# Performance work log

Measured on AMD Instinct MI355X. Metric: run time of the kernel, lower is better.

## Reference

```python
import jax, jax.numpy as jnp
import numpy as np

TEMPERATURE = 0.1
THRESHOLD = 0.2
EPS = 1e-12


def setup_inputs() -> dict:
    key = jax.random.key(0)
    k0, k1 = jax.random.split(key)
    f0 = jax.random.normal(k0, (1, 256, 80, 80), dtype=jnp.float32)
    f1 = jax.random.normal(k1, (1, 256, 80, 80), dtype=jnp.float32)
    return {"f0": f0, "f1": f1}


def reference(f0, f1):
    B, C, H0, W0 = f0.shape
    _, _, H1, W1 = f1.shape
    N0, N1 = H0 * W0, H1 * W1

    # (B, N, C), L2-normalized along C (matches F.normalize with eps clamp)
    f0_flat = f0.reshape(B, C, N0).transpose(0, 2, 1)
    f1_flat = f1.reshape(B, C, N1).transpose(0, 2, 1)
    f0n = f0_flat / jnp.maximum(jnp.linalg.norm(f0_flat, axis=-1, keepdims=True), EPS)
    f1n = f1_flat / jnp.maximum(jnp.linalg.norm(f1_flat, axis=-1, keepdims=True), EPS)

    # cosine similarity / temperature: (B, N0, N1)
    S = jnp.einsum('bnc,bmc->bnm', f0n, f1n) / TEMPERATURE
    # dual softmax
    P = jax.nn.softmax(S, axis=-1) * jax.nn.softmax(S, axis=-2)

    # mutual nearest-neighbor matching (B == 1 branch)
    conf = jnp.max(P[0], axis=-1)              # (N0,)
    indices0 = jnp.argmax(P[0], axis=-1)       # (N0,) row argmax
    indices1 = jnp.argmax(P[0], axis=-2)       # (N1,) column argmax
    ar0 = jnp.arange(N0)
    mutual = indices1[indices0] == ar0
    valid = mutual & (conf > THRESHOLD)        # (N0,) bool

    # fixed-shape (jit-friendly) match outputs: full grid, zeroed where invalid
    mkpts0 = jnp.stack([ar0 % W0, ar0 // W0], axis=1).astype(jnp.float32)
    mkpts1 = jnp.stack([indices0 % W1, indices0 // W1], axis=1).astype(jnp.float32)
    vf = valid[:, None].astype(jnp.float32)
    mkpts0 = mkpts0 * vf
    mkpts1 = mkpts1 * vf
    mconf = jnp.where(valid, conf, 0.0)

    return (P, mkpts0, mkpts1, mconf, valid)
```

## Files before the change

kernel.cpp:

```cpp
#include <hip/hip_runtime.h>

#define N0 6400
#define NC 256
#define WW 80

using half8   = __attribute__((ext_vector_type(8))) _Float16;
using floatx4 = __attribute__((ext_vector_type(4))) float;
#define GLOBAL_AS __attribute__((address_space(1)))
#define LDS_AS    __attribute__((address_space(3)))

__device__ __forceinline__ unsigned long long packvi(float v, int i) {
    return ((unsigned long long)__float_as_uint(v) << 32) | (unsigned int)i;
}

__global__ __launch_bounds__(256) void knorm(const float* __restrict__ f0,
                                             const float* __restrict__ f1,
                                             float* __restrict__ snorm,
                                             float* __restrict__ rowsum,
                                             float* __restrict__ colsum,
                                             unsigned long long* __restrict__ rowbest,
                                             unsigned long long* __restrict__ colbest) {
    int g = blockIdx.x * 256 + threadIdx.x;
    if (g < N0) {
        rowsum[g] = 0.f; colsum[g] = 0.f;
        rowbest[g] = 0ull; colbest[g] = 0ull;
    }
    int h = (g >= 12800) ? 1 : 0;
    int j = g - h * 12800;
    const float* src = (j < N0) ? f0 : f1;
    int n = (j < N0) ? j : (j - N0);
    int c0 = h * 128;
    float s = 0.f;
#pragma unroll 8
    for (int c = 0; c < 128; ++c) {
        float v = src[(c0 + c) * N0 + n];
        s += v * v;
    }
    snorm[g] = s;
}

__global__ __launch_bounds__(256) void ktrans(const float* __restrict__ f0,
                                              const float* __restrict__ f1,
                                              const float* __restrict__ snorm,
                                              _Float16* __restrict__ A2,
                                              _Float16* __restrict__ B2) {
    __shared__ float tile[32][33];
    const float* src = blockIdx.z ? f1 : f0;
    _Float16* dst    = blockIdx.z ? B2 : A2;
    int t = threadIdx.x;
    int n0 = blockIdx.x * 32, c0 = blockIdx.y * 32;
    int tx = t & 31, ty = t >> 5;
#pragma unroll
    for (int u = 0; u < 4; ++u)
        tile[ty + u * 8][tx] = src[(c0 + ty + u * 8) * N0 + n0 + tx];
    __syncthreads();
    int row = t >> 3;
    int cg  = (t & 7) * 4;
    int n = n0 + row;
    int j = (blockIdx.z ? N0 : 0) + n;
    float s = snorm[j] + snorm[12800 + j];
    float iv = 1.0f / fmaxf(sqrtf(s), 1e-12f);
    union { ushort4 u4; _Float16 h[4]; } pk;
#pragma unroll
    for (int u = 0; u < 4; ++u)
        pk.h[u] = (_Float16)(tile[cg + u][row] * iv);
    *(ushort4*)&dst[n * NC + c0 + cg] = pk.u4;
}

__device__ __forceinline__ void stage_chunk(const _Float16* __restrict__ G,
                                            unsigned short* lds, int r0, int kc,
                                            int tid) {
    int rl = tid >> 3;
    int ch = ((tid & 7) ^ (rl & 7)) * 8;
#pragma unroll
    for (int kk = 0; kk < 2; ++kk)
#pragma unroll
        for (int g = 0; g < 4; ++g) {
            const _Float16* ga = G + (r0 + g * 32 + rl) * NC + kc * 128 + kk * 64 + ch;
            __builtin_amdgcn_global_load_lds((const GLOBAL_AS unsigned int*)ga,
                (LDS_AS unsigned int*)&lds[kk * 8192 + g * 2048 + tid * 8], 16, 0, 0);
        }
}

template<bool HI>
__device__ __forceinline__ void compute_half(const unsigned short* bbuf,
                                             const unsigned short* abufHi,
                                             const half8 aflo[4][4],
                                             int lane, int wm, int wn,
                                             floatx4 acc[4][4]) {
    int q = lane >> 4;
#pragma unroll
    for (int s = 0; s < 4; ++s) {
        int c = s * 4 + q, kk = c >> 3, cq = c & 7;
        half8 af[4], bf[4];
#pragma unroll
        for (int mt = 0; mt < 4; ++mt) {
            int rb = wn * 64 + mt * 16 + (lane & 15);
            bf[mt] = *(const half8*)&bbuf[kk * 8192 + rb * 64 + ((cq ^ (rb & 7)) * 8)];
        }
#pragma unroll
        for (int mt = 0; mt < 4; ++mt) {
            if (HI) {
                int ra = wm * 64 + mt * 16 + (lane & 15);
                af[mt] = *(const half8*)&abufHi[kk * 8192 + ra * 64 + ((cq ^ (ra & 7)) * 8)];
            } else {
                af[mt] = aflo[mt][s];
            }
        }
#pragma unroll
        for (int mt = 0; mt < 4; ++mt)
#pragma unroll
            for (int nt = 0; nt < 4; ++nt)
                acc[mt][nt] = __builtin_amdgcn_mfma_f32_16x16x32_f16(
                    af[mt], bf[nt], acc[mt][nt], 0, 0, 0);
    }
}

__global__ __launch_bounds__(256, 2) void kgemm1(const _Float16* __restrict__ A2,
                                                 const _Float16* __restrict__ B2,
                                                 float* __restrict__ rowsum,
                                                 float* __restrict__ colsum) {
    __shared__ __align__(16) unsigned short lds[32768];
    unsigned short* regA = lds;
    unsigned short* regB = lds + 16384;
    int tid = threadIdx.x, lane = tid & 63, wave = tid >> 6;
    int wm = wave & 1, wn = wave >> 1, q = lane >> 4;
    int i0 = blockIdx.x * 128, jp = blockIdx.y * 640;

    stage_chunk(A2, regB, i0, 0, tid);
    stage_chunk(A2, regA, i0, 1, tid);
    __syncthreads();
    half8 aflo[4][4];
#pragma unroll
    for (int mt = 0; mt < 4; ++mt)
#pragma unroll
        for (int s = 0; s < 4; ++s) {
            int c = s * 4 + q, kk = c >> 3, cq = c & 7;
            int ra = wm * 64 + mt * 16 + (lane & 15);
            aflo[mt][s] = *(const half8*)&regB[kk * 8192 + ra * 64 + ((cq ^ (ra & 7)) * 8)];
        }
    __syncthreads();

    float rsum[4][4] = {};

    for (int jt = 0; jt < 5; ++jt) {
        stage_chunk(B2, regB, jp + jt * 128, 0, tid);
        __syncthreads();
        floatx4 acc[4][4] = {};
        compute_half<false>(regB, regA, aflo, lane, wm, wn, acc);
        __syncthreads();
        stage_chunk(B2, regB, jp + jt * 128, 1, tid);
        __syncthreads();
        compute_half<true>(regB, regA, aflo, lane, wm, wn, acc);

        float csum[4] = {0.f, 0.f, 0.f, 0.f};
#pragma unroll
        for (int mt = 0; mt < 4; ++mt)
#pragma unroll
            for (int r = 0; r < 4; ++r) {
                float rv = 0.f;
#pragma unroll
                for (int nt = 0; nt < 4; ++nt) {
                    float e = __expf(10.0f * acc[mt][nt][r]);
                    rv += e; csum[nt] += e;
                }
                rsum[mt][r] += rv;
            }
#pragma unroll
        for (int nt = 0; nt < 4; ++nt) {
            csum[nt] += __shfl_xor(csum[nt], 16);
            csum[nt] += __shfl_xor(csum[nt], 32);
        }
        if (lane < 16)
#pragma unroll
            for (int nt = 0; nt < 4; ++nt)
                atomicAdd(&colsum[jp + jt * 128 + wn * 64 + nt * 16 + lane], csum[nt]);
        __syncthreads();
    }
#pragma unroll
    for (int mt = 0; mt < 4; ++mt)
#pragma unroll
        for (int r = 0; r < 4; ++r) {
            float v = rsum[mt][r];
            v += __shfl_xor(v, 1);
            v += __shfl_xor(v, 2);
            v += __shfl_xor(v, 4);
            v += __shfl_xor(v, 8);
            if ((lane & 15) == 0)
                atomicAdd(&rowsum[i0 + wm * 64 + mt * 16 + q * 4 + r], v);
        }
}

__global__ __launch_bounds__(256, 2) void kgemm2(const _Float16* __restrict__ A2,
                                                 const _Float16* __restrict__ B2,
                                                 const float* __restrict__ rowsum,
                                                 const float* __restrict__ colsum,
                                                 float* __restrict__ P,
                                                 unsigned long long* __restrict__ rowbest,
                                                 unsigned long long* __restrict__ colbest) {
    __shared__ __align__(16) unsigned short lds[32768];
    unsigned short* regA = lds;
    unsigned short* regB = lds + 16384;
    int tid = threadIdx.x, lane = tid & 63, wave = tid >> 6;
    int wm = wave & 1, wn = wave >> 1, q = lane >> 4;
    int i0 = blockIdx.x * 128, jp = blockIdx.y * 640;

    stage_chunk(A2, regB, i0, 0, tid);
    stage_chunk(A2, regA, i0, 1, tid);
    __syncthreads();
    half8 aflo[4][4];
#pragma unroll
    for (int mt = 0; mt < 4; ++mt)
#pragma unroll
        for (int s = 0; s < 4; ++s) {
            int c = s * 4 + q, kk = c >> 3, cq = c & 7;
            int ra = wm * 64 + mt * 16 + (lane & 15);
            aflo[mt][s] = *(const half8*)&regB[kk * 8192 + ra * 64 + ((cq ^ (ra & 7)) * 8)];
        }
    __syncthreads();

    float ir[4][4];
#pragma unroll
    for (int mt = 0; mt < 4; ++mt) {
        float4 v4 = *(const float4*)&rowsum[i0 + wm * 64 + mt * 16 + q * 4];
        ir[mt][0] = 1.0f / v4.x; ir[mt][1] = 1.0f / v4.y;
        ir[mt][2] = 1.0f / v4.z; ir[mt][3] = 1.0f / v4.w;
    }

    unsigned long long rbv[4][4] = {};

    for (int jt = 0; jt < 5; ++jt) {
        stage_chunk(B2, regB, jp + jt * 128, 0, tid);
        __syncthreads();
        floatx4 acc[4][4] = {};
        compute_half<false>(regB, regA, aflo, lane, wm, wn, acc);
        __syncthreads();
        stage_chunk(B2, regB, jp + jt * 128, 1, tid);
        __syncthreads();
        compute_half<true>(regB, regA, aflo, lane, wm, wn, acc);

        int cb0 = jp + jt * 128 + wn * 64 + (lane & 15);
        float ic[4];
#pragma unroll
        for (int nt = 0; nt < 4; ++nt) ic[nt] = 1.0f / colsum[cb0 + nt * 16];

        unsigned long long colb[4] = {0ull, 0ull, 0ull, 0ull};
#pragma unroll
        for (int mt = 0; mt < 4; ++mt) {
            int rb0 = i0 + wm * 64 + mt * 16 + q * 4;
#pragma unroll
            for (int r = 0; r < 4; ++r) {
                int row = rb0 + r;
#pragma unroll
                for (int nt = 0; nt < 4; ++nt) {
                    float pv = __expf(20.0f * acc[mt][nt][r]) * ir[mt][r] * ic[nt];
                    P[row * N0 + cb0 + nt * 16] = pv;
                    unsigned long long pr = packvi(pv, cb0 + nt * 16);
                    if (pr > rbv[mt][r]) rbv[mt][r] = pr;
                    unsigned long long pc = packvi(pv, row);
                    if (pc > colb[nt]) colb[nt] = pc;
                }
            }
        }
#pragma unroll
        for (int nt = 0; nt < 4; ++nt) {
            unsigned long long o = __shfl_xor(colb[nt], 16);
            if (o > colb[nt]) colb[nt] = o;
            o = __shfl_xor(colb[nt], 32);
            if (o > colb[nt]) colb[nt] = o;
        }
        if (lane < 16)
#pragma unroll
            for (int nt = 0; nt < 4; ++nt)
                atomicMax(&colbest[cb0 + nt * 16], colb[nt]);
        __syncthreads();
    }
#pragma unroll
    for (int mt = 0; mt < 4; ++mt)
#pragma unroll
        for (int r = 0; r < 4; ++r) {
            unsigned long long v = rbv[mt][r];
#pragma unroll
            for (int s = 1; s < 16; s <<= 1) {
                unsigned long long o = __shfl_xor(v, s);
                if (o > v) v = o;
            }
            if ((lane & 15) == 0)
                atomicMax(&rowbest[i0 + wm * 64 + mt * 16 + q * 4 + r], v);
        }
}

__global__ __launch_bounds__(256) void kmatch(const unsigned long long* __restrict__ rowbest,
                                              const unsigned long long* __restrict__ colbest,
                                              float* __restrict__ out) {
    int i = blockIdx.x * 256 + threadIdx.x;
    unsigned long long rb = rowbest[i];
    float conf = __uint_as_float((unsigned int)(rb >> 32));
    int jj = (int)(rb & 0xffffffffu);
    unsigned long long cb = colbest[jj];
    int i2 = (int)(cb & 0xffffffffu);
    bool valid = (i2 == i) && (conf > 0.2f);
    float vf = valid ? 1.0f : 0.0f;

    float* mk0   = out + 40960000;
    float* mk1   = out + 40972800;
    float* mconf = out + 40985600;
    float* vout  = out + 40992000;
    mk0[i * 2 + 0] = vf * (float)(i % WW);
    mk0[i * 2 + 1] = vf * (float)(i / WW);
    mk1[i * 2 + 0] = vf * (float)(jj % WW);
    mk1[i * 2 + 1] = vf * (float)(jj / WW);
    mconf[i] = valid ? conf : 0.0f;
    vout[i]  = vf;
}

extern "C" void kernel_launch(void* const* d_in, const int* in_sizes, int n_in,
                              void* d_out, int out_size, void* d_ws, size_t ws_size,
                              hipStream_t stream) {
    const float* f0 = (const float*)d_in[0];
    const float* f1 = (const float*)d_in[1];
    float* out = (float*)d_out;

    _Float16* A2 = (_Float16*)d_ws;
    _Float16* B2 = A2 + 6400 * 256;
    float* snorm  = (float*)(B2 + 6400 * 256);
    float* rowsum = snorm + 25600;
    float* colsum = rowsum + 6400;
    unsigned long long* rowbest = (unsigned long long*)(colsum + 6400);
    unsigned long long* colbest = rowbest + 6400;

    knorm<<<100, 256, 0, stream>>>(f0, f1, snorm,
                                   rowsum, colsum, rowbest, colbest);
    ktrans<<<dim3(200, 8, 2), 256, 0, stream>>>(f0, f1, snorm, A2, B2);
    kgemm1<<<dim3(50, 10), 256, 0, stream>>>(A2, B2, rowsum, colsum);
    kgemm2<<<dim3(50, 10), 256, 0, stream>>>(A2, B2, rowsum, colsum,
                                             out, rowbest, colbest);
    kmatch<<<25, 256, 0, stream>>>(rowbest, colbest, out);
}
```

Baseline: 280.9 us.

## Replace global atomics with per-block partial buffers and a separate reduce pass

Instead of atomicAdd/atomicMax into shared row/col accumulators, each GEMM block reduces within LDS across its waves and writes its own partials to workspace. A small kreduce kernel sums the partials, and the match kernel takes the max over them. The P stores also switch to nontemporal. This removes atomic contention, but it adds an extra launch, extra partial-buffer traffic, and a 50-way strided gather per row in the match kernel. It depends on the workspace being large enough and falls back to the old atomic path otherwise.

```diff
diff --git a/kernel.cpp b/kernel.cpp
--- a/kernel.cpp
+++ b/kernel.cpp
@@ -116,33 +116,43 @@
     }
 }
 
-__global__ __launch_bounds__(256, 2) void kgemm1(const _Float16* __restrict__ A2,
-                                                 const _Float16* __restrict__ B2,
-                                                 float* __restrict__ rowsum,
-                                                 float* __restrict__ colsum) {
+__device__ __forceinline__ void gemm_prologue(const _Float16* __restrict__ A2,
+                                              unsigned short* regA,
+                                              unsigned short* regB,
+                                              int i0, int tid, int lane,
+                                              int wm, half8 aflo[4][4]) {
+    int q = lane >> 4;
+    stage_chunk(A2, regB, i0, 0, tid);
+    stage_chunk(A2, regA, i0, 1, tid);
+    __syncthreads();
+#pragma unroll
+    for (int mt = 0; mt < 4; ++mt)
+#pragma unroll
+        for (int s = 0; s < 4; ++s) {
+            int c = s * 4 + q, kk = c >> 3, cq = c & 7;
+            int ra = wm * 64 + mt * 16 + (lane & 15);
+            aflo[mt][s] = *(const half8*)&regB[kk * 8192 + ra * 64 + ((cq ^ (ra & 7)) * 8)];
+        }
+    __syncthreads();
+}
+
+__global__ __launch_bounds__(256, 2) void kgemm1P(const _Float16* __restrict__ A2,
+                                                  const _Float16* __restrict__ B2,
+                                                  float* __restrict__ rowpart,
+                                                  float* __restrict__ colpart) {
     __shared__ __align__(16) unsigned short lds[32768];
+    __shared__ float cs[2][128];
+    __shared__ float rs[2][128];
     unsigned short* regA = lds;
     unsigned short* regB = lds + 16384;
     int tid = threadIdx.x, lane = tid & 63, wave = tid >> 6;
     int wm = wave & 1, wn = wave >> 1, q = lane >> 4;
     int i0 = blockIdx.x * 128, jp = blockIdx.y * 640;
 
-    stage_chunk(A2, regB, i0, 0, tid);
-    stage_chunk(A2, regA, i0, 1, tid);
-    __syncthreads();
     half8 aflo[4][4];
-#pragma unroll
-    for (int mt = 0; mt < 4; ++mt)
-#pragma unroll
-        for (int s = 0; s < 4; ++s) {
-            int c = s * 4 + q, kk = c >> 3, cq = c & 7;
-            int ra = wm * 64 + mt * 16 + (lane & 15);
-            aflo[mt][s] = *(const half8*)&regB[kk * 8192 + ra * 64 + ((cq ^ (ra & 7)) * 8)];
-        }
-    __syncthreads();
+    gemm_prologue(A2, regA, regB, i0, tid, lane, wm, aflo);
 
     float rsum[4][4] = {};
-
     for (int jt = 0; jt < 5; ++jt) {
         stage_chunk(B2, regB, jp + jt * 128, 0, tid);
         __syncthreads();
@@ -174,8 +184,10 @@
         if (lane < 16)
 #pragma unroll
             for (int nt = 0; nt < 4; ++nt)
-                atomicAdd(&colsum[jp + jt * 128 + wn * 64 + nt * 16 + lane], csum[nt]);
-        __syncthreads();
+                cs[wm][wn * 64 + nt * 16 + lane] = csum[nt];
+        __syncthreads();
+        if (tid < 128)
+            colpart[blockIdx.x * N0 + jp + jt * 128 + tid] = cs[0][tid] + cs[1][tid];
     }
 #pragma unroll
     for (int mt = 0; mt < 4; ++mt)
@@ -187,37 +199,50 @@
             v += __shfl_xor(v, 4);
             v += __shfl_xor(v, 8);
             if ((lane & 15) == 0)
-                atomicAdd(&rowsum[i0 + wm * 64 + mt * 16 + q * 4 + r], v);
-        }
-}
-
-__global__ __launch_bounds__(256, 2) void kgemm2(const _Float16* __restrict__ A2,
-                                                 const _Float16* __restrict__ B2,
-                                                 const float* __restrict__ rowsum,
-                                                 const float* __restrict__ colsum,
-                                                 float* __restrict__ P,
-                                                 unsigned long long* __restrict__ rowbest,
-                                                 unsigned long long* __restrict__ colbest) {
+                rs[wn][wm * 64 + mt * 16 + q * 4 + r] = v;
+        }
+    __syncthreads();
+    if (tid < 128)
+        rowpart[blockIdx.y * N0 + i0 + tid] = rs[0][tid] + rs[1][tid];
+}
+
+__global__ __launch_bounds__(256) void kreduce(const float* __restrict__ rowpart,
+                                               const float* __restrict__ colpart,
+                                               float* __restrict__ rowsum,
+                                               float* __restrict__ colsum) {
+    int t = blockIdx.x * 256 + threadIdx.x;
+    if (t < N0) {
+        float s = 0.f;
+#pragma unroll
+        for (int y = 0; y < 10; ++y) s += rowpart[y * N0 + t];
+        rowsum[t] = s;
+    } else {
+        int j = t - N0;
+        float s = 0.f;
+#pragma unroll
+        for (int x = 0; x < 50; ++x) s += colpart[x * N0 + j];
+        colsum[j] = s;
+    }
+}
+
+__global__ __launch_bounds__(256, 2) void kgemm2P(const _Float16* __restrict__ A2,
+                                                  const _Float16* __restrict__ B2,
+                                                  const float* __restrict__ rowsum,
+                                                  const float* __restrict__ colsum,
+                                                  float* __restrict__ P,
+                                                  unsigned long long* __restrict__ rowbpart,
+                                                  unsigned long long* __restrict__ colbpart) {
     __shared__ __align__(16) unsigned short lds[32768];
+    __shared__ unsigned long long cbst[2][128];
+    __shared__ unsigned long long rbst[2][128];
     unsigned short* regA = lds;
     unsigned short* regB = lds + 16384;
     int tid = threadIdx.x, lane = tid & 63, wave = tid >> 6;
     int wm = wave & 1, wn = wave >> 1, q = lane >> 4;
     int i0 = blockIdx.x * 128, jp = blockIdx.y * 640;
 
-    stage_chunk(A2, regB, i0, 0, tid);
-    stage_chunk(A2, regA, i0, 1, tid);
-    __syncthreads();
     half8 aflo[4][4];
-#pragma unroll
-    for (int mt = 0; mt < 4; ++mt)
-#pragma unroll
-        for (int s = 0; s < 4; ++s) {
-            int c = s * 4 + q, kk = c >> 3, cq = c & 7;
-            int ra = wm * 64 + mt * 16 + (lane & 15);
-            aflo[mt][s] = *(const half8*)&regB[kk * 8192 + ra * 64 + ((cq ^ (ra & 7)) * 8)];
-        }
-    __syncthreads();
+    gemm_prologue(A2, regA, regB, i0, tid, lane, wm, aflo);
 
     float ir[4][4];
 #pragma unroll
@@ -228,7 +253,6 @@
     }
 
     unsigned long long rbv[4][4] = {};
-
     for (int jt = 0; jt < 5; ++jt) {
         stage_chunk(B2, regB, jp + jt * 128, 0, tid);
         __syncthreads();
@@ -254,7 +278,7 @@
 #pragma unroll
                 for (int nt = 0; nt < 4; ++nt) {
                     float pv = __expf(20.0f * acc[mt][nt][r]) * ir[mt][r] * ic[nt];
-                    P[row * N0 + cb0 + nt * 16] = pv;
+                    __builtin_nontemporal_store(pv, &P[row * N0 + cb0 + nt * 16]);
                     unsigned long long pr = packvi(pv, cb0 + nt * 16);
                     if (pr > rbv[mt][r]) rbv[mt][r] = pr;
                     unsigned long long pc = packvi(pv, row);
@@ -272,8 +296,12 @@
         if (lane < 16)
 #pragma unroll
             for (int nt = 0; nt < 4; ++nt)
-                atomicMax(&colbest[cb0 + nt * 16], colb[nt]);
-        __syncthreads();
+                cbst[wm][wn * 64 + nt * 16 + lane] = colb[nt];
+        __syncthreads();
+        if (tid < 128) {
+            unsigned long long a = cbst[0][tid], b = cbst[1][tid];
+            colbpart[blockIdx.x * N0 + jp + jt * 128 + tid] = (a > b) ? a : b;
+        }
     }
 #pragma unroll
     for (int mt = 0; mt < 4; ++mt)
@@ -286,18 +314,32 @@
                 if (o > v) v = o;
             }
             if ((lane & 15) == 0)
-                atomicMax(&rowbest[i0 + wm * 64 + mt * 16 + q * 4 + r], v);
-        }
-}
-
-__global__ __launch_bounds__(256) void kmatch(const unsigned long long* __restrict__ rowbest,
-                                              const unsigned long long* __restrict__ colbest,
-                                              float* __restrict__ out) {
+                rbst[wn][wm * 64 + mt * 16 + q * 4 + r] = v;
+        }
+    __syncthreads();
+    if (tid < 128) {
+        unsigned long long a = rbst[0][tid], b = rbst[1][tid];
+        rowbpart[blockIdx.y * N0 + i0 + tid] = (a > b) ? a : b;
+    }
+}
+
+__global__ __launch_bounds__(256) void kmatchP(const unsigned long long* __restrict__ rowbpart,
+                                               const unsigned long long* __restrict__ colbpart,
+                                               float* __restrict__ out) {
     int i = blockIdx.x * 256 + threadIdx.x;
-    unsigned long long rb = rowbest[i];
+    unsigned long long rb = 0ull;
+#pragma unroll
+    for (int y = 0; y < 10; ++y) {
+        unsigned long long v = rowbpart[y * N0 + i];
+        if (v > rb) rb = v;
+    }
     float conf = __uint_as_float((unsigned int)(rb >> 32));
     int jj = (int)(rb & 0xffffffffu);
-    unsigned long long cb = colbest[jj];
+    unsigned long long cb = 0ull;
+    for (int x = 0; x < 50; ++x) {
+        unsigned long long v = colbpart[x * N0 + jj];
+        if (v > cb) cb = v;
+    }
     int i2 = (int)(cb & 0xffffffffu);
     bool valid = (i2 == i) && (conf > 0.2f);
     float vf = valid ? 1.0f : 0.0f;
@@ -314,6 +356,180 @@
     vout[i]  = vf;
 }
 
+__global__ __launch_bounds__(256, 2) void kgemm1A(const _Float16* __restrict__ A2,
+                                                  const _Float16* __restrict__ B2,
+                                                  float* __restrict__ rowsum,
+                                                  float* __restrict__ colsum) {
+    __shared__ __align__(16) unsigned short lds[32768];
+    unsigned short* regA = lds;
+    unsigned short* regB = lds + 16384;
+    int tid = threadIdx.x, lane = tid & 63, wave = tid >> 6;
+    int wm = wave & 1, wn = wave >> 1, q = lane >> 4;
+    int i0 = blockIdx.x * 128, jp = blockIdx.y * 640;
+
+    half8 aflo[4][4];
+    gemm_prologue(A2, regA, regB, i0, tid, lane, wm, aflo);
+
+    float rsum[4][4] = {};
+    for (int jt = 0; jt < 5; ++jt) {
+        stage_chunk(B2, regB, jp + jt * 128, 0, tid);
+        __syncthreads();
+        floatx4 acc[4][4] = {};
+        compute_half<false>(regB, regA, aflo, lane, wm, wn, acc);
+        __syncthreads();
+        stage_chunk(B2, regB, jp + jt * 128, 1, tid);
+        __syncthreads();
+        compute_half<true>(regB, regA, aflo, lane, wm, wn, acc);
+
+        float csum[4] = {0.f, 0.f, 0.f, 0.f};
+#pragma unroll
+        for (int mt = 0; mt < 4; ++mt)
+#pragma unroll
+            for (int r = 0; r < 4; ++r) {
+                float rv = 0.f;
+#pragma unroll
+                for (int nt = 0; nt < 4; ++nt) {
+                    float e = __expf(10.0f * acc[mt][nt][r]);
+                    rv += e; csum[nt] += e;
+                }
+                rsum[mt][r] += rv;
+            }
+#pragma unroll
+        for (int nt = 0; nt < 4; ++nt) {
+            csum[nt] += __shfl_xor(csum[nt], 16);
+            csum[nt] += __shfl_xor(csum[nt], 32);
+        }
+        if (lane < 16)
+#pragma unroll
+            for (int nt = 0; nt < 4; ++nt)
+                atomicAdd(&colsum[jp + jt * 128 + wn * 64 + nt * 16 + lane], csum[nt]);
+        __syncthreads();
+    }
+#pragma unroll
+    for (int mt = 0; mt < 4; ++mt)
+#pragma unroll
+        for (int r = 0; r < 4; ++r) {
+            float v = rsum[mt][r];
+            v += __shfl_xor(v, 1);
+            v += __shfl_xor(v, 2);
+            v += __shfl_xor(v, 4);
+            v += __shfl_xor(v, 8);
+            if ((lane & 15) == 0)
+                atomicAdd(&rowsum[i0 + wm * 64 + mt * 16 + q * 4 + r], v);
+        }
+}
+
+__global__ __launch_bounds__(256, 2) void kgemm2A(const _Float16* __restrict__ A2,
+                                                  const _Float16* __restrict__ B2,
+                                                  const float* __restrict__ rowsum,
+                                                  const float* __restrict__ colsum,
+                                                  float* __restrict__ P,
+                                                  unsigned long long* __restrict__ rowbest,
+                                                  unsigned long long* __restrict__ colbest) {
+    __shared__ __align__(16) unsigned short lds[32768];
+    unsigned short* regA = lds;
+    unsigned short* regB = lds + 16384;
+    int tid = threadIdx.x, lane = tid & 63, wave = tid >> 6;
+    int wm = wave & 1, wn = wave >> 1, q = lane >> 4;
+    int i0 = blockIdx.x * 128, jp = blockIdx.y * 640;
+
+    half8 aflo[4][4];
+    gemm_prologue(A2, regA, regB, i0, tid, lane, wm, aflo);
+
+    float ir[4][4];
+#pragma unroll
+    for (int mt = 0; mt < 4; ++mt) {
+        float4 v4 = *(const float4*)&rowsum[i0 + wm * 64 + mt * 16 + q * 4];
+        ir[mt][0] = 1.0f / v4.x; ir[mt][1] = 1.0f / v4.y;
+        ir[mt][2] = 1.0f / v4.z; ir[mt][3] = 1.0f / v4.w;
+    }
+
+    unsigned long long rbv[4][4] = {};
+    for (int jt = 0; jt < 5; ++jt) {
+        stage_chunk(B2, regB, jp + jt * 128, 0, tid);
+        __syncthreads();
+        floatx4 acc[4][4] = {};
+        compute_half<false>(regB, regA, aflo, lane, wm, wn, acc);
+        __syncthreads();
+        stage_chunk(B2, regB, jp + jt * 128, 1, tid);
+        __syncthreads();
+        compute_half<true>(regB, regA, aflo, lane, wm, wn, acc);
+
+        int cb0 = jp + jt * 128 + wn * 64 + (lane & 15);
+        float ic[4];
+#pragma unroll
+        for (int nt = 0; nt < 4; ++nt) ic[nt] = 1.0f / colsum[cb0 + nt * 16];
+
+        unsigned long long colb[4] = {0ull, 0ull, 0ull, 0ull};
+#pragma unroll
+        for (int mt = 0; mt < 4; ++mt) {
+            int rb0 = i0 + wm * 64 + mt * 16 + q * 4;
+#pragma unroll
+            for (int r = 0; r < 4; ++r) {
+                int row = rb0 + r;
+#pragma unroll
+                for (int nt = 0; nt < 4; ++nt) {
+                    float pv = __expf(20.0f * acc[mt][nt][r]) * ir[mt][r] * ic[nt];
+                    P[row * N0 + cb0 + nt * 16] = pv;
+                    unsigned long long pr = packvi(pv, cb0 + nt * 16);
+                    if (pr > rbv[mt][r]) rbv[mt][r] = pr;
+                    unsigned long long pc = packvi(pv, row);
+                    if (pc > colb[nt]) colb[nt] = pc;
+                }
+            }
+        }
+#pragma unroll
+        for (int nt = 0; nt < 4; ++nt) {
+            unsigned long long o = __shfl_xor(colb[nt], 16);
+            if (o > colb[nt]) colb[nt] = o;
+            o = __shfl_xor(colb[nt], 32);
+            if (o > colb[nt]) colb[nt] = o;
+        }
+        if (lane < 16)
+#pragma unroll
+            for (int nt = 0; nt < 4; ++nt)
+                atomicMax(&colbest[cb0 + nt * 16], colb[nt]);
+        __syncthreads();
+    }
+#pragma unroll
+    for (int mt = 0; mt < 4; ++mt)
+#pragma unroll
+        for (int r = 0; r < 4; ++r) {
+            unsigned long long v = rbv[mt][r];
+#pragma unroll
+            for (int s = 1; s < 16; s <<= 1) {
+                unsigned long long o = __shfl_xor(v, s);
+                if (o > v) v = o;
+            }
+            if ((lane & 15) == 0)
+                atomicMax(&rowbest[i0 + wm * 64 + mt * 16 + q * 4 + r], v);
+        }
+}
+
+__global__ __launch_bounds__(256) void kmatchA(const unsigned long long* __restrict__ rowbest,
+                                               const unsigned long long* __restrict__ colbest,
+                                               float* __restrict__ out) {
+    int i = blockIdx.x * 256 + threadIdx.x;
+    unsigned long long rb = rowbest[i];
+    float conf = __uint_as_float((unsigned int)(rb >> 32));
+    int jj = (int)(rb & 0xffffffffu);
+    unsigned long long cb = colbest[jj];
+    int i2 = (int)(cb & 0xffffffffu);
+    bool valid = (i2 == i) && (conf > 0.2f);
+    float vf = valid ? 1.0f : 0.0f;
+
+    float* mk0   = out + 40960000;
+    float* mk1   = out + 40972800;
+    float* mconf = out + 40985600;
+    float* vout  = out + 40992000;
+    mk0[i * 2 + 0] = vf * (float)(i % WW);
+    mk0[i * 2 + 1] = vf * (float)(i / WW);
+    mk1[i * 2 + 0] = vf * (float)(jj % WW);
+    mk1[i * 2 + 1] = vf * (float)(jj / WW);
+    mconf[i] = valid ? conf : 0.0f;
+    vout[i]  = vf;
+}
+
 extern "C" void kernel_launch(void* const* d_in, const int* in_sizes, int n_in,
                               void* d_out, int out_size, void* d_ws, size_t ws_size,
                               hipStream_t stream) {
@@ -323,17 +539,32 @@
 
     _Float16* A2 = (_Float16*)d_ws;
     _Float16* B2 = A2 + 6400 * 256;
-    float* snorm  = (float*)(B2 + 6400 * 256);
-    float* rowsum = snorm + 25600;
-    float* colsum = rowsum + 6400;
+    float* snorm   = (float*)(B2 + 6400 * 256);
+    float* rowsum  = snorm + 25600;
+    float* colsum  = rowsum + 6400;
     unsigned long long* rowbest = (unsigned long long*)(colsum + 6400);
     unsigned long long* colbest = rowbest + 6400;
+    float* rowpart = (float*)(colbest + 6400);
+    float* colpart = rowpart + 10 * 6400;
+    unsigned long long* rowbpart =
+        (unsigned long long*)(colpart + 50 * 6400);
+    unsigned long long* colbpart = rowbpart + 10 * 6400;
+    const size_t WS_NEEDED_P = 11417600;
 
     knorm<<<100, 256, 0, stream>>>(f0, f1, snorm,
                                    rowsum, colsum, rowbest, colbest);
     ktrans<<<dim3(200, 8, 2), 256, 0, stream>>>(f0, f1, snorm, A2, B2);
-    kgemm1<<<dim3(50, 10), 256, 0, stream>>>(A2, B2, rowsum, colsum);
-    kgemm2<<<dim3(50, 10), 256, 0, stream>>>(A2, B2, rowsum, colsum,
-                                             out, rowbest, colbest);
-    kmatch<<<25, 256, 0, stream>>>(rowbest, colbest, out);
-}
+
+    if (ws_size >= WS_NEEDED_P) {
+        kgemm1P<<<dim3(50, 10), 256, 0, stream>>>(A2, B2, rowpart, colpart);
+        kreduce<<<50, 256, 0, stream>>>(rowpart, colpart, rowsum, colsum);
+        kgemm2P<<<dim3(50, 10), 256, 0, stream>>>(A2, B2, rowsum, colsum,
+                                                  out, rowbpart, colbpart);
+        kmatchP<<<25, 256, 0, stream>>>(rowbpart, colbpart, out);
+    } else {
+        kgemm1A<<<dim3(50, 10), 256, 0, stream>>>(A2, B2, rowsum, colsum);
+        kgemm2A<<<dim3(50, 10), 256, 0, stream>>>(A2, B2, rowsum, colsum,
+                                                  out, rowbest, colbest);
+        kmatchA<<<25, 256, 0, stream>>>(rowbest, colbest, out);
+    }
+}
```

Measured after the change: 294.3 us. 4.8% more time.

## Replace global atomics with partial buffers, log-domain argmax, and coalesced P stores

Applied to the files above, without the earlier changes.

Global atomicAdd/atomicMax reductions of row/column sums and best indices are replaced by per-block partial arrays, combined by a new reduce kernel and inside the match kernel. The argmax keys move to the log domain (S plus log normalizers), so P values no longer need packing, and conf is read back from P. The P writes go through a per-wave LDS scratch to form 16-byte coalesced nontemporal stores instead of strided scalar stores. This adds one kernel launch and extra partial-buffer traffic, and log-domain ties could pick a different index than comparing exact P values.

```diff
diff --git a/kernel.cpp b/kernel.cpp
--- a/kernel.cpp
+++ b/kernel.cpp
@@ -15,16 +15,8 @@
 
 __global__ __launch_bounds__(256) void knorm(const float* __restrict__ f0,
                                              const float* __restrict__ f1,
-                                             float* __restrict__ snorm,
-                                             float* __restrict__ rowsum,
-                                             float* __restrict__ colsum,
-                                             unsigned long long* __restrict__ rowbest,
-                                             unsigned long long* __restrict__ colbest) {
+                                             float* __restrict__ snorm) {
     int g = blockIdx.x * 256 + threadIdx.x;
-    if (g < N0) {
-        rowsum[g] = 0.f; colsum[g] = 0.f;
-        rowbest[g] = 0ull; colbest[g] = 0ull;
-    }
     int h = (g >= 12800) ? 1 : 0;
     int j = g - h * 12800;
     const float* src = (j < N0) ? f0 : f1;
@@ -116,33 +108,43 @@
     }
 }
 
-__global__ __launch_bounds__(256, 2) void kgemm1(const _Float16* __restrict__ A2,
-                                                 const _Float16* __restrict__ B2,
-                                                 float* __restrict__ rowsum,
-                                                 float* __restrict__ colsum) {
+__device__ __forceinline__ void gemm_prologue(const _Float16* __restrict__ A2,
+                                              unsigned short* regA,
+                                              unsigned short* regB,
+                                              int i0, int tid, int lane,
+                                              int wm, half8 aflo[4][4]) {
+    int q = lane >> 4;
+    stage_chunk(A2, regB, i0, 0, tid);
+    stage_chunk(A2, regA, i0, 1, tid);
+    __syncthreads();
+#pragma unroll
+    for (int mt = 0; mt < 4; ++mt)
+#pragma unroll
+        for (int s = 0; s < 4; ++s) {
+            int c = s * 4 + q, kk = c >> 3, cq = c & 7;
+            int ra = wm * 64 + mt * 16 + (lane & 15);
+            aflo[mt][s] = *(const half8*)&regB[kk * 8192 + ra * 64 + ((cq ^ (ra & 7)) * 8)];
+        }
+    __syncthreads();
+}
+
+__global__ __launch_bounds__(256, 2) void kgemm1P(const _Float16* __restrict__ A2,
+                                                  const _Float16* __restrict__ B2,
+                                                  float* __restrict__ rowpart,
+                                                  float* __restrict__ colpart) {
     __shared__ __align__(16) unsigned short lds[32768];
+    __shared__ float cs[2][128];
+    __shared__ float rs[2][128];
     unsigned short* regA = lds;
     unsigned short* regB = lds + 16384;
     int tid = threadIdx.x, lane = tid & 63, wave = tid >> 6;
     int wm = wave & 1, wn = wave >> 1, q = lane >> 4;
     int i0 = blockIdx.x * 128, jp = blockIdx.y * 640;
 
-    stage_chunk(A2, regB, i0, 0, tid);
-    stage_chunk(A2, regA, i0, 1, tid);
-    __syncthreads();
     half8 aflo[4][4];
-#pragma unroll
-    for (int mt = 0; mt < 4; ++mt)
-#pragma unroll
-        for (int s = 0; s < 4; ++s) {
-            int c = s * 4 + q, kk = c >> 3, cq = c & 7;
-            int ra = wm * 64 + mt * 16 + (lane & 15);
-            aflo[mt][s] = *(const half8*)&regB[kk * 8192 + ra * 64 + ((cq ^ (ra & 7)) * 8)];
-        }
-    __syncthreads();
+    gemm_prologue(A2, regA, regB, i0, tid, lane, wm, aflo);
 
     float rsum[4][4] = {};
-
     for (int jt = 0; jt < 5; ++jt) {
         stage_chunk(B2, regB, jp + jt * 128, 0, tid);
         __syncthreads();
@@ -174,8 +176,10 @@
         if (lane < 16)
 #pragma unroll
             for (int nt = 0; nt < 4; ++nt)
-                atomicAdd(&colsum[jp + jt * 128 + wn * 64 + nt * 16 + lane], csum[nt]);
-        __syncthreads();
+                cs[wm][wn * 64 + nt * 16 + lane] = csum[nt];
+        __syncthreads();
+        if (tid < 128)
+            colpart[blockIdx.x * N0 + jp + jt * 128 + tid] = cs[0][tid] + cs[1][tid];
     }
 #pragma unroll
     for (int mt = 0; mt < 4; ++mt)
@@ -187,48 +191,65 @@
             v += __shfl_xor(v, 4);
             v += __shfl_xor(v, 8);
             if ((lane & 15) == 0)
-                atomicAdd(&rowsum[i0 + wm * 64 + mt * 16 + q * 4 + r], v);
-        }
-}
-
-__global__ __launch_bounds__(256, 2) void kgemm2(const _Float16* __restrict__ A2,
-                                                 const _Float16* __restrict__ B2,
-                                                 const float* __restrict__ rowsum,
-                                                 const float* __restrict__ colsum,
-                                                 float* __restrict__ P,
-                                                 unsigned long long* __restrict__ rowbest,
-                                                 unsigned long long* __restrict__ colbest) {
+                rs[wn][wm * 64 + mt * 16 + q * 4 + r] = v;
+        }
+    __syncthreads();
+    if (tid < 128)
+        rowpart[blockIdx.y * N0 + i0 + tid] = rs[0][tid] + rs[1][tid];
+}
+
+__global__ __launch_bounds__(256) void kreduce(const float* __restrict__ rowpart,
+                                               const float* __restrict__ colpart,
+                                               float* __restrict__ rowsum,
+                                               float* __restrict__ colsum) {
+    int t = blockIdx.x * 256 + threadIdx.x;
+    if (t < N0) {
+        float s = 0.f;
+#pragma unroll
+        for (int y = 0; y < 10; ++y) s += rowpart[y * N0 + t];
+        rowsum[t] = s;
+    } else {
+        int j = t - N0;
+        float s = 0.f;
+#pragma unroll
+        for (int x = 0; x < 50; ++x) s += colpart[x * N0 + j];
+        colsum[j] = s;
+    }
+}
+
+__global__ __launch_bounds__(256, 2) void kgemm2P(const _Float16* __restrict__ A2,
+                                                  const _Float16* __restrict__ B2,
+                                                  const float* __restrict__ rowsum,
+                                                  const float* __restrict__ colsum,
+                                                  float* __restrict__ P,
+                                                  unsigned long long* __restrict__ rowbpart,
+                                                  unsigned long long* __restrict__ colbpart) {
     __shared__ __align__(16) unsigned short lds[32768];
+    __shared__ unsigned long long cbst[2][128];
+    __shared__ unsigned long long rbst[2][128];
     unsigned short* regA = lds;
     unsigned short* regB = lds + 16384;
     int tid = threadIdx.x, lane = tid & 63, wave = tid >> 6;
     int wm = wave & 1, wn = wave >> 1, q = lane >> 4;
     int i0 = blockIdx.x * 128, jp = blockIdx.y * 640;
 
-    stage_chunk(A2, regB, i0, 0, tid);
-    stage_chunk(A2, regA, i0, 1, tid);
-    __syncthreads();
     half8 aflo[4][4];
-#pragma unroll
-    for (int mt = 0; mt < 4; ++mt)
-#pragma unroll
-        for (int s = 0; s < 4; ++s) {
-            int c = s * 4 + q, kk = c >> 3, cq = c & 7;
-            int ra = wm * 64 + mt * 16 + (lane & 15);
-            aflo[mt][s] = *(const half8*)&regB[kk * 8192 + ra * 64 + ((cq ^ (ra & 7)) * 8)];
-        }
-    __syncthreads();
-
-    float ir[4][4];
+    gemm_prologue(A2, regA, regB, i0, tid, lane, wm, aflo);
+
+    float ir[4][4], lr[4][4];
 #pragma unroll
     for (int mt = 0; mt < 4; ++mt) {
         float4 v4 = *(const float4*)&rowsum[i0 + wm * 64 + mt * 16 + q * 4];
         ir[mt][0] = 1.0f / v4.x; ir[mt][1] = 1.0f / v4.y;
         ir[mt][2] = 1.0f / v4.z; ir[mt][3] = 1.0f / v4.w;
-    }
+#pragma unroll
+        for (int r = 0; r < 4; ++r)
+            lr[mt][r] = __logf(ir[mt][r]) * 0.05f + 4.0f;
+    }
+
+    float* scr = (float*)lds + 8192 + wave * 1056;
 
     unsigned long long rbv[4][4] = {};
-
     for (int jt = 0; jt < 5; ++jt) {
         stage_chunk(B2, regB, jp + jt * 128, 0, tid);
         __syncthreads();
@@ -239,10 +260,14 @@
         __syncthreads();
         compute_half<true>(regB, regA, aflo, lane, wm, wn, acc);
 
-        int cb0 = jp + jt * 128 + wn * 64 + (lane & 15);
-        float ic[4];
-#pragma unroll
-        for (int nt = 0; nt < 4; ++nt) ic[nt] = 1.0f / colsum[cb0 + nt * 16];
+        int jcb = jp + jt * 128 + wn * 64;
+        int cb0 = jcb + (lane & 15);
+        float ic[4], lc[4];
+#pragma unroll
+        for (int nt = 0; nt < 4; ++nt) {
+            ic[nt] = 1.0f / colsum[cb0 + nt * 16];
+            lc[nt] = __logf(ic[nt]) * 0.05f + 4.0f;
+        }
 
         unsigned long long colb[4] = {0ull, 0ull, 0ull, 0ull};
 #pragma unroll
@@ -251,15 +276,23 @@
 #pragma unroll
             for (int r = 0; r < 4; ++r) {
                 int row = rb0 + r;
+                float lrr = lr[mt][r];
 #pragma unroll
                 for (int nt = 0; nt < 4; ++nt) {
-                    float pv = __expf(20.0f * acc[mt][nt][r]) * ir[mt][r] * ic[nt];
-                    P[row * N0 + cb0 + nt * 16] = pv;
-                    unsigned long long pr = packvi(pv, cb0 + nt * 16);
+                    float a  = acc[mt][nt][r];
+                    float pv = __expf(20.0f * a) * ir[mt][r] * ic[nt];
+                    scr[(q * 4 + r) * 66 + (lane & 15) + nt * 16] = pv;
+                    unsigned long long pr = packvi(a + lc[nt], cb0 + nt * 16);
                     if (pr > rbv[mt][r]) rbv[mt][r] = pr;
-                    unsigned long long pc = packvi(pv, row);
+                    unsigned long long pc = packvi(a + lrr, row);
                     if (pc > colb[nt]) colb[nt] = pc;
                 }
+            }
+#pragma unroll
+            for (int g = 0; g < 4; ++g) {
+                floatx4 o = *(const floatx4*)&scr[(g * 4 + (lane >> 4)) * 66 + (lane & 15) * 4];
+                int row = i0 + wm * 64 + mt * 16 + g * 4 + (lane >> 4);
+                __builtin_nontemporal_store(o, (floatx4*)&P[row * N0 + jcb + (lane & 15) * 4]);
             }
         }
 #pragma unroll
@@ -272,8 +305,12 @@
         if (lane < 16)
 #pragma unroll
             for (int nt = 0; nt < 4; ++nt)
-                atomicMax(&colbest[cb0 + nt * 16], colb[nt]);
-        __syncthreads();
+                cbst[wm][wn * 64 + nt * 16 + lane] = colb[nt];
+        __syncthreads();
+        if (tid < 128) {
+            unsigned long long a = cbst[0][tid], b = cbst[1][tid];
+            colbpart[blockIdx.x * N0 + jp + jt * 128 + tid] = (a > b) ? a : b;
+        }
     }
 #pragma unroll
     for (int mt = 0; mt < 4; ++mt)
@@ -286,19 +323,34 @@
                 if (o > v) v = o;
             }
             if ((lane & 15) == 0)
-                atomicMax(&rowbest[i0 + wm * 64 + mt * 16 + q * 4 + r], v);
-        }
-}
-
-__global__ __launch_bounds__(256) void kmatch(const unsigned long long* __restrict__ rowbest,
-                                              const unsigned long long* __restrict__ colbest,
-                                              float* __restrict__ out) {
+                rbst[wn][wm * 64 + mt * 16 + q * 4 + r] = v;
+        }
+    __syncthreads();
+    if (tid < 128) {
+        unsigned long long a = rbst[0][tid], b = rbst[1][tid];
+        rowbpart[blockIdx.y * N0 + i0 + tid] = (a > b) ? a : b;
+    }
+}
+
+__global__ __launch_bounds__(256) void kmatchP(const unsigned long long* __restrict__ rowbpart,
+                                               const unsigned long long* __restrict__ colbpart,
+                                               const float* __restrict__ P,
+                                               float* __restrict__ out) {
     int i = blockIdx.x * 256 + threadIdx.x;
-    unsigned long long rb = rowbest[i];
-    float conf = __uint_as_float((unsigned int)(rb >> 32));
+    unsigned long long rb = 0ull;
+#pragma unroll
+    for (int y = 0; y < 10; ++y) {
+        unsigned long long v = rowbpart[y * N0 + i];
+        if (v > rb) rb = v;
+    }
     int jj = (int)(rb & 0xffffffffu);
-    unsigned long long cb = colbest[jj];
+    unsigned long long cb = 0ull;
+    for (int x = 0; x < 50; ++x) {
+        unsigned long long v = colbpart[x * N0 + jj];
+        if (v > cb) cb = v;
+    }
     int i2 = (int)(cb & 0xffffffffu);
+    float conf = P[i * N0 + jj];
     bool valid = (i2 == i) && (conf > 0.2f);
     float vf = valid ? 1.0f : 0.0f;
 
@@ -323,17 +375,20 @@
 
     _Float16* A2 = (_Float16*)d_ws;
     _Float16* B2 = A2 + 6400 * 256;
-    float* snorm  = (float*)(B2 + 6400 * 256);
-    float* rowsum = snorm + 25600;
-    float* colsum = rowsum + 6400;
-    unsigned long long* rowbest = (unsigned long long*)(colsum + 6400);
-    unsigned long long* colbest = rowbest + 6400;
-
-    knorm<<<100, 256, 0, stream>>>(f0, f1, snorm,
-                                   rowsum, colsum, rowbest, colbest);
+    float* snorm   = (float*)(B2 + 6400 * 256);
+    float* rowsum  = snorm + 25600;
+    float* colsum  = rowsum + 6400;
+    float* rowpart = colsum + 6400;
+    float* colpart = rowpart + 10 * 6400;
+    unsigned long long* rowbpart =
+        (unsigned long long*)(colpart + 50 * 6400);
+    unsigned long long* colbpart = rowbpart + 10 * 6400;
+
+    knorm<<<100, 256, 0, stream>>>(f0, f1, snorm);
     ktrans<<<dim3(200, 8, 2), 256, 0, stream>>>(f0, f1, snorm, A2, B2);
-    kgemm1<<<dim3(50, 10), 256, 0, stream>>>(A2, B2, rowsum, colsum);
-    kgemm2<<<dim3(50, 10), 256, 0, stream>>>(A2, B2, rowsum, colsum,
-                                             out, rowbest, colbest);
-    kmatch<<<25, 256, 0, stream>>>(rowbest, colbest, out);
-}
+    kgemm1P<<<dim3(50, 10), 256, 0, stream>>>(A2, B2, rowpart, colpart);
+    kreduce<<<50, 256, 0, stream>>>(rowpart, colpart, rowsum, colsum);
+    kgemm2P<<<dim3(50, 10), 256, 0, stream>>>(A2, B2, rowsum, colsum,
+                                              out, rowbpart, colbpart);
+    kmatchP<<<25, 256, 0, stream>>>(rowbpart, colbpart, out, out);
+}
```

Measured after the change: 285.0 us. No clear change (+1.4%).
